# Performance work log

Measured on AMD Instinct MI355X. Metric: run time of the kernel, lower is better.

## Reference

```python
import jax, jax.numpy as jnp
import numpy as np
from jax import lax

B, T, D, E, N, P, S, NCLS, NBLK = 64, 16384, 128, 256, 8, 16, 1024, 18, 3
EPS = 1e-5


def setup_inputs() -> dict:
    key = jax.random.key(0)
    ks = jax.random.split(key, 20)
    inp = {
        'inputs': jax.random.normal(ks[0], (B, T, 6), jnp.float32),
        'acc_w': jax.random.normal(ks[1], (D // 2, 3, P), jnp.float32) * 0.1,
        'acc_b': jnp.zeros((D // 2,), jnp.float32),
        'gyro_w': jax.random.normal(ks[2], (D // 2, 3, P), jnp.float32) * 0.1,
        'gyro_b': jnp.zeros((D // 2,), jnp.float32),
        'pos_emb': jax.random.normal(ks[3], (S, D), jnp.float32),
        'ln_g': jnp.ones((NBLK, D), jnp.float32),
        'ln_b': jnp.zeros((NBLK, D), jnp.float32),
        'pc1_w': jax.random.normal(ks[4], (NBLK, E, D), jnp.float32) * 0.05,
        'pc1_b': jnp.zeros((NBLK, E), jnp.float32),
        'dw_w': jax.random.normal(ks[5], (NBLK, E, 5), jnp.float32) * 0.1,
        'dw_b': jnp.zeros((NBLK, E), jnp.float32),
        'bn_g': jnp.ones((NBLK, E), jnp.float32),
        'bn_b': jnp.zeros((NBLK, E), jnp.float32),
        'bn_mean': jnp.zeros((NBLK, E), jnp.float32),
        'bn_var': jnp.ones((NBLK, E), jnp.float32),
        'Ap': -0.5 * jnp.ones((NBLK, E), jnp.float32),
        'Bp': jax.random.normal(ks[6], (NBLK, E, N), jnp.float32) * 0.1,
        'Cp': jax.random.normal(ks[7], (NBLK, E, N), jnp.float32) * 0.1,
        'Dp': jax.random.normal(ks[8], (NBLK, E), jnp.float32) * 0.1,
        'pc2_w': jax.random.normal(ks[9], (NBLK, D, E), jnp.float32) * 0.05,
        'pc2_b': jnp.zeros((NBLK, D), jnp.float32),
        'fln_g': jnp.ones((D,), jnp.float32),
        'fln_b': jnp.zeros((D,), jnp.float32),
        'hw1': jax.random.normal(ks[10], (D, 2 * D), jnp.float32) * 0.05,
        'hb1': jnp.zeros((2 * D,), jnp.float32),
        'hw2': jax.random.normal(ks[11], (2 * D, NCLS), jnp.float32) * 0.05,
        'hb2': jnp.zeros((NCLS,), jnp.float32),
    }
    return inp


def _layernorm(x, g, b):
    m = x.mean(-1, keepdims=True)
    v = ((x - m) ** 2).mean(-1, keepdims=True)
    return (x - m) * lax.rsqrt(v + EPS) * g + b


def _conv1d(x, w, b, stride):
    # x [B,C,L], w [O,I,K]
    y = lax.conv_general_dilated(x, w, (stride,), 'VALID',
                                 dimension_numbers=('NCH', 'OIH', 'NCH'))
    return y + b[None, :, None]


def _mamba(x, pc1_w, pc1_b, dw_w, dw_b, bn_g, bn_b, bn_mean, bn_var,
           Ap, Bp, Cp, Dp, pc2_w, pc2_b):
    # x: [B,S,D]
    xc = jax.nn.silu(jnp.einsum('bsd,ed->bse', x, pc1_w) + pc1_b)  # [B,S,E]
    xt = jnp.swapaxes(xc, 1, 2)  # [B,E,S]
    # depthwise conv k=5, pad=2, groups=E
    xl = lax.conv_general_dilated(xt, dw_w[:, None, :], (1,), [(2, 2)],
                                  feature_group_count=E,
                                  dimension_numbers=('NCH', 'OIH', 'NCH'))
    xl = xl + dw_b[None, :, None]
    # BatchNorm1d (eval mode, running stats)
    scale = bn_g * lax.rsqrt(bn_var + EPS)
    xl = (xl - bn_mean[None, :, None]) * scale[None, :, None] + bn_b[None, :, None]
    xl = jax.nn.silu(xl)
    x_local = jnp.swapaxes(xl, 1, 2)  # [B,S,E]
    # SSM scan: h = exp(A)*h + x_t * B ; y = sum(C*h) + D*x_t
    A_exp = jnp.exp(Ap)  # [E]

    def step(h, xt_):
        # h [B,E,N], xt_ [B,E]
        h = A_exp[None, :, None] * h + xt_[..., None] * Bp[None]
        y = jnp.einsum('ben,en->be', h, Cp) + Dp * xt_
        return h, y

    h0 = jnp.zeros((x_local.shape[0], E, N), x_local.dtype)
    _, ys = lax.scan(step, h0, jnp.swapaxes(x_local, 0, 1))  # ys [S,B,E]
    out = jnp.swapaxes(ys, 0, 1)  # [B,S,E]
    out = jnp.einsum('bse,de->bsd', out, pc2_w) + pc2_b
    return out


def reference(inputs, acc_w, acc_b, gyro_w, gyro_b, pos_emb,
              ln_g, ln_b, pc1_w, pc1_b, dw_w, dw_b, bn_g, bn_b, bn_mean, bn_var,
              Ap, Bp, Cp, Dp, pc2_w, pc2_b, fln_g, fln_b, hw1, hb1, hw2, hb2):
    acc = jnp.swapaxes(inputs[:, :, :3], 1, 2)   # [B,3,T]
    gyro = jnp.swapaxes(inputs[:, :, 3:], 1, 2)  # [B,3,T]
    acc_p = jnp.swapaxes(_conv1d(acc, acc_w, acc_b, 16), 1, 2)    # [B,S,D/2]
    gyro_p = jnp.swapaxes(_conv1d(gyro, gyro_w, gyro_b, 16), 1, 2)
    x = jnp.concatenate([acc_p, gyro_p], axis=2)  # [B,S,D]
    x = x + pos_emb[None]
    for i in range(NBLK):
        y = _layernorm(x, ln_g[i], ln_b[i])
        y = _mamba(y, pc1_w[i], pc1_b[i], dw_w[i], dw_b[i], bn_g[i], bn_b[i],
                   bn_mean[i], bn_var[i], Ap[i], Bp[i], Cp[i], Dp[i],
                   pc2_w[i], pc2_b[i])
        x = y + x
    x = _layernorm(x, fln_g, fln_b)
    x = x.mean(axis=1)  # [B,D]
    h = jax.nn.silu(x @ hw1 + hb1)
    logits = h @ hw2 + hb2
    return jax.nn.softmax(logits, axis=-1)
```

## Files before the change

kernel.cpp:

```cpp
#include <hip/hip_runtime.h>
#include <hip/hip_bf16.h>

#define BB 64
#define TT 16384
#define DD 128
#define EE 256
#define NN 8
#define SS 1024
#define NCLS 18
#define NBLK 3
#define EPSV 1e-5f

typedef __bf16 bf16x8 __attribute__((ext_vector_type(8)));
typedef __bf16 bf16x4 __attribute__((ext_vector_type(4)));
typedef float f32x4 __attribute__((ext_vector_type(4)));
typedef unsigned short ushort_t;

__device__ __forceinline__ float silu_f(float z) {
    return z * __builtin_amdgcn_rcpf(1.0f + __expf(-z));
}
__device__ __forceinline__ unsigned int bfbits(float v) {
    return (unsigned int)__builtin_bit_cast(unsigned short, (__bf16)v);
}
__device__ __forceinline__ float bflow(unsigned int u) {
    return (float)__builtin_bit_cast(__bf16, (unsigned short)(u & 0xffffu));
}
__device__ __forceinline__ float bfhigh(unsigned int u) {
    return (float)__builtin_bit_cast(__bf16, (unsigned short)(u >> 16));
}

__global__ __launch_bounds__(256) void k_pack(
    const float* __restrict__ w1, const float* __restrict__ w2,
    const float* __restrict__ dw_w, const float* __restrict__ dw_b,
    const float* __restrict__ bn_g, const float* __restrict__ bn_b,
    const float* __restrict__ bn_mean, const float* __restrict__ bn_var,
    const float* __restrict__ Ap, const float* __restrict__ Bp,
    const float* __restrict__ Cp, const float* __restrict__ Dp,
    ushort_t* __restrict__ wpk1, ushort_t* __restrict__ wpk2,
    float* __restrict__ sparm) {
    const int t0 = blockIdx.x * 256 + threadIdx.x;
    if (t0 >= 24576) {
        const int t = t0 - 24576;
        if (t >= 768) return;
        const int le = t;
        const float scale = bn_g[le] * rsqrtf(bn_var[le] + EPSV);
        float cb = 0.0f;
#pragma unroll
        for (int n = 0; n < 8; ++n) cb += Cp[le * 8 + n] * Bp[le * 8 + n];
        float* dst = sparm + (size_t)le * 12;
        dst[0] = dw_w[le * 5 + 0] * scale;
        dst[1] = dw_w[le * 5 + 1] * scale;
        dst[2] = dw_w[le * 5 + 2] * scale;
        dst[3] = dw_w[le * 5 + 3] * scale;
        dst[4] = dw_w[le * 5 + 4] * scale;
        dst[5] = (dw_b[le] - bn_mean[le]) * scale + bn_b[le];
        dst[6] = __expf(Ap[le]);
        dst[7] = cb;
        dst[8] = Dp[le];
        dst[9] = 0.0f; dst[10] = 0.0f; dst[11] = 0.0f;
        return;
    }
    const float* src;
    uint4* dst;
    if (t0 < 12288) {
        const int L = t0 >> 12;
        const int r = t0 & 4095;
        const int ks = r >> 10;
        const int r2 = r & 1023;
        const int nf = r2 >> 6;
        const int lane = r2 & 63;
        const int col = nf * 16 + (lane & 15);
        const int k0 = ks * 32 + (lane >> 4) * 8;
        src = w1 + ((size_t)L * EE + col) * DD + k0;
        dst = (uint4*)wpk1 + t0;
    } else {
        const int t = t0 - 12288;
        const int L = t >> 12;
        const int r = t & 4095;
        const int ks = r >> 9;
        const int r2 = r & 511;
        const int nf = r2 >> 6;
        const int lane = r2 & 63;
        const int col = nf * 16 + (lane & 15);
        const int k0 = ks * 32 + (lane >> 4) * 8;
        src = w2 + ((size_t)L * DD + col) * EE + k0;
        dst = (uint4*)wpk2 + t;
    }
    const float4 a = ((const float4*)src)[0];
    const float4 b = ((const float4*)src)[1];
    bf16x8 pk;
    pk[0] = (__bf16)a.x; pk[1] = (__bf16)a.y; pk[2] = (__bf16)a.z; pk[3] = (__bf16)a.w;
    pk[4] = (__bf16)b.x; pk[5] = (__bf16)b.y; pk[6] = (__bf16)b.z; pk[7] = (__bf16)b.w;
    *dst = __builtin_bit_cast(uint4, pk);
}

__device__ __forceinline__ void xt_store(ushort_t* xt16, int row, int col,
                                         ushort_t val) {
    xt16[row * 128 + (((col >> 3) ^ (row & 7)) << 3) + (col & 7)] = val;
}

template <int MROWS, int NT>
__device__ __forceinline__ void ln_pc1_tail(
    char* smem, const int tid,
    const float* __restrict__ lng, const float* __restrict__ lnb,
    const ushort_t* __restrict__ wpk, const float* __restrict__ bias1,
    __bf16* __restrict__ xcT, const int bidx, const int sg0) {
    constexpr int TPR = NT / MROWS;
    constexpr int CPT = 16 / TPR;
    const uint4* xt = (const uint4*)smem;
    uint4* A2 = (uint4*)(smem + MROWS * 256);

    {
        const int row = tid / TPR;
        const int q = tid % TPR;
        float v[CPT * 8];
#pragma unroll
        for (int i = 0; i < CPT; ++i) {
            const uint4 tv4 = xt[row * 16 + ((q * CPT + i) ^ (row & 7))];
            const bf16x8 tv = __builtin_bit_cast(bf16x8, tv4);
#pragma unroll
            for (int e2 = 0; e2 < 8; ++e2) v[i * 8 + e2] = (float)tv[e2];
        }
        float s1 = 0.0f, s2 = 0.0f;
#pragma unroll
        for (int i = 0; i < CPT * 8; ++i) { s1 += v[i]; s2 += v[i] * v[i]; }
        s1 += __shfl_xor(s1, 1); s2 += __shfl_xor(s2, 1);
        s1 += __shfl_xor(s1, 2); s2 += __shfl_xor(s2, 2);
        const float mean = s1 * (1.0f / 128.0f);
        const float rstd = rsqrtf(s2 * (1.0f / 128.0f) - mean * mean + EPSV);
        const float4* gp4 = (const float4*)lng;
        const float4* bp4 = (const float4*)lnb;
#pragma unroll
        for (int c = 0; c < CPT; ++c) {
            const int ci = q * CPT + c;
            float4 g0 = gp4[ci * 2], g1 = gp4[ci * 2 + 1];
            float4 b0 = bp4[ci * 2], b1 = bp4[ci * 2 + 1];
            const float gg[8] = {g0.x, g0.y, g0.z, g0.w, g1.x, g1.y, g1.z, g1.w};
            const float bb2[8] = {b0.x, b0.y, b0.z, b0.w, b1.x, b1.y, b1.z, b1.w};
            bf16x8 pk;
#pragma unroll
            for (int e2 = 0; e2 < 8; ++e2)
                pk[e2] = (__bf16)((v[c * 8 + e2] - mean) * rstd * gg[e2] + bb2[e2]);
            A2[(row * 16 + ci) ^ (row & 7)] = __builtin_bit_cast(uint4, pk);
        }
    }
    __syncthreads();

    const int wv = tid >> 6;
    const int wr = wv >> 2;
    const int wc = wv & 3;
    const int lane = tid & 63;
    const int lrow = lane & 15;
    const int lk = lane >> 4;
    const uint4* wq = (const uint4*)wpk;

    f32x4 acc[4][4] = {};
    for (int ks = 0; ks < 4; ++ks) {
        bf16x8 av[4], bw[4];
#pragma unroll
        for (int m = 0; m < 4; ++m) {
            const int row = wr * 64 + m * 16 + lrow;
            const int idx = (row * 16 + ks * 4 + lk) ^ (row & 7);
            av[m] = __builtin_bit_cast(bf16x8, A2[idx]);
        }
#pragma unroll
        for (int n = 0; n < 4; ++n) {
            const int nf = wc * 4 + n;
            bw[n] = __builtin_bit_cast(bf16x8, wq[(ks * 16 + nf) * 64 + lane]);
        }
#pragma unroll
        for (int m = 0; m < 4; ++m)
#pragma unroll
            for (int n = 0; n < 4; ++n)
                acc[m][n] = __builtin_amdgcn_mfma_f32_16x16x32_bf16(av[m], bw[n], acc[m][n], 0, 0, 0);
    }

#pragma unroll
    for (int n = 0; n < 4; ++n) {
        const int col = wc * 64 + n * 16 + lrow;
        const float bv = bias1[col];
#pragma unroll
        for (int m = 0; m < 4; ++m) {
            bf16x4 pk;
#pragma unroll
            for (int r = 0; r < 4; ++r)
                pk[r] = (__bf16)silu_f(acc[m][n][r] + bv);
            const int sg = sg0 + wr * 8 + m * 2 + (lk >> 1);
            __bf16* dst = xcT + ((((size_t)bidx * 128 + sg) * EE + col) << 3) +
                          (lk & 1) * 4;
            *(bf16x4*)dst = pk;
        }
    }
}

__global__ __launch_bounds__(256) void k_stem_mfma(
    const float* __restrict__ in, const float* __restrict__ acc_w,
    const float* __restrict__ acc_b, const float* __restrict__ gyro_w,
    const float* __restrict__ gyro_b, const float* __restrict__ pos_emb,
    __bf16* __restrict__ x,
    const float* __restrict__ lng, const float* __restrict__ lnb,
    const ushort_t* __restrict__ wpk1, const float* __restrict__ pc1b,
    __bf16* __restrict__ xcT) {
    __shared__ __align__(16) char smem[49152];
    uint4* Wl = (uint4*)smem;
    uint4* Al = (uint4*)(smem + 32768);

    const int tid = threadIdx.x;
    const int rbase = blockIdx.x * 64;
    const int b = rbase >> 10;
    const int sbase = rbase & 1023;

    if (tid < 128) {
        const int d = tid;
        const float* wsrc = (d < 64) ? (acc_w + d * 48) : (gyro_w + (d - 64) * 48);
        float aw[48];
        const float4* wq4 = (const float4*)wsrc;
#pragma unroll
        for (int q = 0; q < 12; ++q) {
            float4 t = wq4[q];
            aw[q * 4 + 0] = t.x; aw[q * 4 + 1] = t.y;
            aw[q * 4 + 2] = t.z; aw[q * 4 + 3] = t.w;
        }
        const bool isacc = (d < 64);
#pragma unroll
        for (int cc = 0; cc < 12; ++cc) {
            unsigned int wb[8];
#pragma unroll
            for (int e = 0; e < 8; ++e) {
                const int j = cc * 8 + e;
                const int p = j / 6, rem = j % 6;
                float val;
                if (rem < 3) val = isacc ? aw[rem * 16 + p] : 0.0f;
                else         val = isacc ? 0.0f : aw[(rem - 3) * 16 + p];
                wb[e] = bfbits(val);
            }
            uint4 pk;
            pk.x = wb[0] | (wb[1] << 16);
            pk.y = wb[2] | (wb[3] << 16);
            pk.z = wb[4] | (wb[5] << 16);
            pk.w = wb[6] | (wb[7] << 16);
            Wl[d * 16 + (cc ^ (d & 7))] = pk;
        }
    }

    {
        const float* abase = in + (size_t)b * (TT * 6) + (size_t)sbase * 96;
#pragma unroll
        for (int it = 0; it < 3; ++it) {
            const int idx = it * 256 + tid;
            const int row = idx / 12;
            const int ch = idx % 12;
            const float* src = abase + row * 96 + ch * 8;
            const float4 t0 = *(const float4*)src;
            const float4 t1 = *(const float4*)(src + 4);
            uint4 pk;
            pk.x = bfbits(t0.x) | (bfbits(t0.y) << 16);
            pk.y = bfbits(t0.z) | (bfbits(t0.w) << 16);
            pk.z = bfbits(t1.x) | (bfbits(t1.y) << 16);
            pk.w = bfbits(t1.z) | (bfbits(t1.w) << 16);
            Al[row * 16 + (ch ^ (row & 7))] = pk;
        }
    }
    __syncthreads();

    const int wv = tid >> 6;
    const int lane = tid & 63;
    const int lrow = lane & 15;
    const int lk = lane >> 4;

    f32x4 acc[4][2] = {};
#pragma unroll
    for (int ks = 0; ks < 3; ++ks) {
        bf16x8 a[4], bf[2];
#pragma unroll
        for (int m = 0; m < 4; ++m) {
            const int row = m * 16 + lrow;
            a[m] = __builtin_bit_cast(bf16x8, Al[row * 16 + ((ks * 4 + lk) ^ (row & 7))]);
        }
#pragma unroll
        for (int n = 0; n < 2; ++n) {
            const int col = (wv * 2 + n) * 16 + lrow;
            bf[n] = __builtin_bit_cast(bf16x8, Wl[col * 16 + ((ks * 4 + lk) ^ (col & 7))]);
        }
#pragma unroll
        for (int m = 0; m < 4; ++m)
#pragma unroll
            for (int n = 0; n < 2; ++n)
                acc[m][n] = __builtin_amdgcn_mfma_f32_16x16x32_bf16(a[m], bf[n], acc[m][n], 0, 0, 0);
    }
    __syncthreads();

    ushort_t* xt16 = (ushort_t*)smem;
#pragma unroll
    for (int n = 0; n < 2; ++n) {
        const int col = (wv * 2 + n) * 16 + lrow;
        const float bv = (col < 64) ? acc_b[col] : gyro_b[col - 64];
#pragma unroll
        for (int m = 0; m < 4; ++m)
#pragma unroll
            for (int r = 0; r < 4; ++r) {
                const int row = m * 16 + lk * 4 + r;
                const float pe = pos_emb[(size_t)(sbase + row) * DD + col];
                const float xv = acc[m][n][r] + bv + pe;
                const __bf16 xb = (__bf16)xv;
                x[(size_t)(rbase + row) * DD + col] = xb;
                xt_store(xt16, row, col, __builtin_bit_cast(ushort_t, xb));
            }
    }
    __syncthreads();
    ln_pc1_tail<64, 256>(smem, tid, lng, lnb, wpk1, pc1b, xcT, b, sbase >> 3);
}

template <int TAIL>
__global__ __launch_bounds__(512, 4) void k_scan_pc2(
    const __bf16* __restrict__ xcIn,
    const ushort_t* __restrict__ wpk2_,
    const float* __restrict__ sparm,
    const float* __restrict__ bias, __bf16* __restrict__ x,
    const float* __restrict__ lng, const float* __restrict__ lnb,
    const ushort_t* __restrict__ wpk1, const float* __restrict__ pc1b,
    __bf16* __restrict__ xcOut) {
    __shared__ __align__(16) char smem[65536];

    const int tid = threadIdx.x;
    const int sc = blockIdx.x;
    const int b = blockIdx.y;

    {
        const int e = tid & 255;
        const int sub = tid >> 8;
        const int sce = sc * 2 + sub;
        const float4 p0 = *(const float4*)(sparm + (size_t)e * 12);
        const float4 p1 = *(const float4*)(sparm + (size_t)e * 12 + 4);
        const float Dv = sparm[(size_t)e * 12 + 8];
        const float d0 = p0.x, d1 = p0.y, d2 = p0.z, d3 = p0.w;
        const float d4 = p1.x, cbias = p1.y, Aexp = p1.z, cb = p1.w;

        const int sgbase = sce * 8 - 4;
        const uint4* xq = (const uint4*)xcIn + ((size_t)b * 128 + sgbase) * EE + e;
        uint4 G[13];
#pragma unroll
        for (int j = 0; j < 13; ++j) {
            const int sg = sgbase + j;
            G[j] = (sg >= 0 && sg < 128) ? xq[j * EE] : make_uint4(0, 0, 0, 0);
        }

        __bf16* lbase = (__bf16*)smem;
        const int ehash = e >> 3;
        const int elow = e & 7;
        const int rowoff = sub * 64;

        float g = 0.0f, pw6, pw7;
        if (sce != 0) {
            pw6 = bflow(G[0].w); pw7 = bfhigh(G[0].w);
#pragma unroll
            for (int j = 1; j <= 3; ++j) {
                float cw[8];
                cw[0] = bflow(G[j].x); cw[1] = bfhigh(G[j].x);
                cw[2] = bflow(G[j].y); cw[3] = bfhigh(G[j].y);
                cw[4] = bflow(G[j].z); cw[5] = bfhigh(G[j].z);
                cw[6] = bflow(G[j].w); cw[7] = bfhigh(G[j].w);
                const float nh0 = bflow(G[j + 1].x);
                const float nh1 = bfhigh(G[j + 1].x);
#pragma unroll
                for (int u = 0; u < 8; ++u) {
                    const float xm2 = (u >= 2) ? cw[u - 2] : (u == 0 ? pw6 : pw7);
                    const float xm1 = (u >= 1) ? cw[u - 1] : pw7;
                    const float x0 = cw[u];
                    const float xp1 = (u < 7) ? cw[u + 1] : nh0;
                    const float xp2 = (u < 6) ? cw[u + 2] : (u == 6 ? nh0 : nh1);
                    const float z = xm2 * d0 + xm1 * d1 + x0 * d2 + xp1 * d3 +
                                    xp2 * d4 + cbias;
                    g = fmaf(Aexp, g, silu_f(z));
                }
                pw6 = cw[6]; pw7 = cw[7];
            }
        } else {
            pw6 = 0.0f; pw7 = 0.0f;
        }

#pragma unroll
        for (int j = 4; j <= 11; ++j) {
            float cw[8];
            cw[0] = bflow(G[j].x); cw[1] = bfhigh(G[j].x);
            cw[2] = bflow(G[j].y); cw[3] = bfhigh(G[j].y);
            cw[4] = bflow(G[j].z); cw[5] = bfhigh(G[j].z);
            cw[6] = bflow(G[j].w); cw[7] = bfhigh(G[j].w);
            const float nh0 = bflow(G[j + 1].x);
            const float nh1 = bfhigh(G[j + 1].x);

            float aa[8];
#pragma unroll
            for (int u = 0; u < 8; ++u) {
                const float xm2 = (u >= 2) ? cw[u - 2] : (u == 0 ? pw6 : pw7);
                const float xm1 = (u >= 1) ? cw[u - 1] : pw7;
                const float x0 = cw[u];
                const float xp1 = (u < 7) ? cw[u + 1] : nh0;
                const float xp2 = (u < 6) ? cw[u + 2] : (u == 6 ? nh0 : nh1);
                const float z = xm2 * d0 + xm1 * d1 + x0 * d2 + xp1 * d3 +
                                xp2 * d4 + cbias;
                aa[u] = silu_f(z);
            }
#pragma unroll
            for (int u = 0; u < 8; ++u) {
                g = fmaf(Aexp, g, aa[u]);
                const int r = rowoff + (j - 4) * 8 + u;
                lbase[r * 256 + ((ehash ^ (r & 7)) << 3) + elow] =
                    (__bf16)(cb * g + Dv * aa[u]);
            }
            pw6 = cw[6]; pw7 = cw[7];
        }
    }
    __syncthreads();

    const size_t rbase = ((size_t)b << 10) + ((size_t)sc << 7);
    const int wv = tid >> 6;
    const int wr = wv >> 2;
    const int wc = wv & 3;
    const int lane = tid & 63;
    const int lrow = lane & 15;
    const int lk = lane >> 4;
    const uint4* wq = (const uint4*)wpk2_;
    const uint4* Albd = (const uint4*)smem;

    f32x4 acc[4][2] = {};
    for (int ks = 0; ks < 8; ++ks) {
        bf16x8 a[4], bfr[2];
#pragma unroll
        for (int m = 0; m < 4; ++m) {
            const int row = wr * 64 + m * 16 + lrow;
            const int idx = (row * 32 + ks * 4 + lk) ^ (row & 7);
            a[m] = __builtin_bit_cast(bf16x8, Albd[idx]);
        }
#pragma unroll
        for (int n = 0; n < 2; ++n) {
            const int nf = wc * 2 + n;
            bfr[n] = __builtin_bit_cast(bf16x8, wq[(ks * 8 + nf) * 64 + lane]);
        }
#pragma unroll
        for (int m = 0; m < 4; ++m)
#pragma unroll
            for (int n = 0; n < 2; ++n)
                acc[m][n] = __builtin_amdgcn_mfma_f32_16x16x32_bf16(a[m], bfr[n], acc[m][n], 0, 0, 0);
    }
    if constexpr (TAIL) __syncthreads();

    ushort_t* xt16 = (ushort_t*)smem;
#pragma unroll
    for (int n = 0; n < 2; ++n) {
        const int col = wc * 32 + n * 16 + lrow;
        const float bv = bias[col];
#pragma unroll
        for (int m = 0; m < 4; ++m)
#pragma unroll
            for (int r = 0; r < 4; ++r) {
                const int row = wr * 64 + m * 16 + lk * 4 + r;
                __bf16* xp = x + (rbase + row) * DD + col;
                const float xn = (float)*xp + acc[m][n][r] + bv;
                const __bf16 xb = (__bf16)xn;
                *xp = xb;
                if constexpr (TAIL)
                    xt_store(xt16, row, col, __builtin_bit_cast(ushort_t, xb));
            }
    }
    if constexpr (TAIL) {
        __syncthreads();
        ln_pc1_tail<128, 512>(smem, tid, lng, lnb, wpk1, pc1b, xcOut, b, sc * 16);
    }
}

__global__ __launch_bounds__(256) void k_finln_s1(
    const __bf16* __restrict__ x, float* __restrict__ partial) {
    const int chunk = blockIdx.x;
    const int b = blockIdx.y;
    const int tid = threadIdx.x;
    const int wv = tid >> 6;
    const int lane = tid & 63;
    const __bf16* xb = x + ((size_t)b * SS + chunk * 128) * DD;

    float a0 = 0.0f, a1 = 0.0f;
    for (int s = wv; s < 128; s += 4) {
        const unsigned int vv = *(const unsigned int*)(xb + (size_t)s * DD + lane * 2);
        const float vx = bflow(vv);
        const float vy = bfhigh(vv);
        float s1 = vx + vy;
        float s2 = vx * vx + vy * vy;
#pragma unroll
        for (int m = 1; m <= 32; m <<= 1) {
            s1 += __shfl_xor(s1, m);
            s2 += __shfl_xor(s2, m);
        }
        const float mean = s1 * (1.0f / 128.0f);
        const float rstd = rsqrtf(s2 * (1.0f / 128.0f) - mean * mean + EPSV);
        a0 += (vx - mean) * rstd;
        a1 += (vy - mean) * rstd;
    }
    __shared__ float red[4][128];
    red[wv][lane * 2] = a0;
    red[wv][lane * 2 + 1] = a1;
    __syncthreads();
    if (tid < 128) {
        partial[((size_t)b * 8 + chunk) * 128 + tid] =
            red[0][tid] + red[1][tid] + red[2][tid] + red[3][tid];
    }
}

__global__ __launch_bounds__(256) void k_head(
    const float* __restrict__ partial, const float* __restrict__ fg,
    const float* __restrict__ fb, const float* __restrict__ hw1,
    const float* __restrict__ hb1, const float* __restrict__ hw2,
    const float* __restrict__ hb2, float* __restrict__ out) {
    const int b = blockIdx.x;
    const int tid = threadIdx.x;
    __shared__ float xmb[128];
    __shared__ float hh[256];
    __shared__ float lg[18];
    __shared__ float eg[18];

    if (tid < 128) {
        float s = 0.0f;
#pragma unroll
        for (int c = 0; c < 8; ++c)
            s += partial[((size_t)b * 8 + c) * 128 + tid];
        xmb[tid] = fg[tid] * (s * (1.0f / (float)SS)) + fb[tid];
    }
    __syncthreads();

    float z = hb1[tid];
    for (int k = 0; k < 128; ++k) z += xmb[k] * hw1[k * 256 + tid];
    hh[tid] = z / (1.0f + expf(-z));
    __syncthreads();

    if (tid < NCLS) {
        float a = hb2[tid];
        for (int k = 0; k < 256; ++k) a += hh[k] * hw2[k * NCLS + tid];
        lg[tid] = a;
    }
    __syncthreads();
    if (tid < NCLS) {
        float m = lg[0];
        for (int j = 1; j < NCLS; ++j) m = fmaxf(m, lg[j]);
        eg[tid] = expf(lg[tid] - m);
    }
    __syncthreads();
    if (tid < NCLS) {
        float ssum = 0.0f;
        for (int j = 0; j < NCLS; ++j) ssum += eg[j];
        out[b * NCLS + tid] = eg[tid] / ssum;
    }
}

extern "C" void kernel_launch(void* const* d_in, const int* in_sizes, int n_in,
                              void* d_out, int out_size, void* d_ws, size_t ws_size,
                              hipStream_t stream) {
    const float* inputs  = (const float*)d_in[0];
    const float* acc_w   = (const float*)d_in[1];
    const float* acc_b   = (const float*)d_in[2];
    const float* gyro_w  = (const float*)d_in[3];
    const float* gyro_b  = (const float*)d_in[4];
    const float* pos_emb = (const float*)d_in[5];
    const float* ln_g    = (const float*)d_in[6];
    const float* ln_b    = (const float*)d_in[7];
    const float* pc1_w   = (const float*)d_in[8];
    const float* pc1_b   = (const float*)d_in[9];
    const float* dw_w    = (const float*)d_in[10];
    const float* dw_b    = (const float*)d_in[11];
    const float* bn_g    = (const float*)d_in[12];
    const float* bn_b    = (const float*)d_in[13];
    const float* bn_mean = (const float*)d_in[14];
    const float* bn_var  = (const float*)d_in[15];
    const float* Ap      = (const float*)d_in[16];
    const float* Bp      = (const float*)d_in[17];
    const float* Cp      = (const float*)d_in[18];
    const float* Dp      = (const float*)d_in[19];
    const float* pc2_w   = (const float*)d_in[20];
    const float* pc2_b   = (const float*)d_in[21];
    const float* fln_g   = (const float*)d_in[22];
    const float* fln_b   = (const float*)d_in[23];
    const float* hw1     = (const float*)d_in[24];
    const float* hb1     = (const float*)d_in[25];
    const float* hw2     = (const float*)d_in[26];
    const float* hb2     = (const float*)d_in[27];

    const size_t nx  = (size_t)BB * SS * DD;
    const size_t nxc = (size_t)BB * SS * EE;

    ushort_t* wsu = (ushort_t*)d_ws;
    ushort_t* xb   = wsu;
    ushort_t* xc0  = xb + nx;
    ushort_t* xc1  = xc0 + nxc;
    ushort_t* wpk1 = xc1 + nxc;
    ushort_t* wpk2 = wpk1 + 3 * 32768;
    float* sparm   = (float*)(wpk2 + 3 * 32768);
    float* partial = sparm + 3 * 256 * 12;

    __bf16* x    = (__bf16*)xb;
    __bf16* xcT0 = (__bf16*)xc0;
    __bf16* xcT1 = (__bf16*)xc1;

    k_pack<<<99, 256, 0, stream>>>(pc1_w, pc2_w, dw_w, dw_b, bn_g, bn_b,
                                   bn_mean, bn_var, Ap, Bp, Cp, Dp,
                                   wpk1, wpk2, sparm);

    k_stem_mfma<<<1024, 256, 0, stream>>>(inputs, acc_w, acc_b, gyro_w, gyro_b,
                                          pos_emb, x,
                                          ln_g, ln_b, wpk1, pc1_b, xcT0);

    k_scan_pc2<1><<<dim3(8, BB), 512, 0, stream>>>(
        xcT0, wpk2, sparm,
        pc2_b, x,
        ln_g + DD, ln_b + DD, wpk1 + 32768, pc1_b + EE, xcT1);

    k_scan_pc2<1><<<dim3(8, BB), 512, 0, stream>>>(
        xcT1, wpk2 + 32768, sparm + 256 * 12,
        pc2_b + DD, x,
        ln_g + 2 * DD, ln_b + 2 * DD, wpk1 + 2 * 32768, pc1_b + 2 * EE, xcT0);

    k_scan_pc2<0><<<dim3(8, BB), 512, 0, stream>>>(
        xcT0, wpk2 + 2 * 32768, sparm + 2 * 256 * 12,
        pc2_b + 2 * DD, x,
        nullptr, nullptr, nullptr, nullptr, nullptr);

    k_finln_s1<<<dim3(8, BB), 256, 0, stream>>>(x, partial);
    k_head<<<BB, 256, 0, stream>>>(partial, fln_g, fln_b, hw1, hb1, hw2, hb2,
                                   (float*)d_out);
}
```

Measured before the change: 153.8 us.

## Fuse per-layer LN, pc1, scan and pc2 into one kernel with recomputed halo

Each block now loads its 128-row chunk of x plus a 32-row halo, and computes layernorm and the pc1 GEMM itself. It then runs the depthwise conv and scan on pc1 output kept in shared memory, and applies pc2 with the residual, writing to a ping-pong x buffer. This removes the global xcT intermediate (B*S*E bf16 written and read per layer) and drops the LN/pc1 tail from the stem and previous layer. In exchange the halo rows are recomputed for pc1 and the scan warmup. Shared memory grows to about 124KB per block, which lowers occupancy, and the scan runs in serialized 32-row steps separated by barriers.

Result: slower. 257.6 us (+67.4%).

```diff
diff --git a/kernel.cpp b/kernel.cpp
--- a/kernel.cpp
+++ b/kernel.cpp
@@ -94,113 +94,11 @@
     *dst = __builtin_bit_cast(uint4, pk);
 }
 
-__device__ __forceinline__ void xt_store(ushort_t* xt16, int row, int col,
-                                         ushort_t val) {
-    xt16[row * 128 + (((col >> 3) ^ (row & 7)) << 3) + (col & 7)] = val;
-}
-
-template <int MROWS, int NT>
-__device__ __forceinline__ void ln_pc1_tail(
-    char* smem, const int tid,
-    const float* __restrict__ lng, const float* __restrict__ lnb,
-    const ushort_t* __restrict__ wpk, const float* __restrict__ bias1,
-    __bf16* __restrict__ xcT, const int bidx, const int sg0) {
-    constexpr int TPR = NT / MROWS;
-    constexpr int CPT = 16 / TPR;
-    const uint4* xt = (const uint4*)smem;
-    uint4* A2 = (uint4*)(smem + MROWS * 256);
-
-    {
-        const int row = tid / TPR;
-        const int q = tid % TPR;
-        float v[CPT * 8];
-#pragma unroll
-        for (int i = 0; i < CPT; ++i) {
-            const uint4 tv4 = xt[row * 16 + ((q * CPT + i) ^ (row & 7))];
-            const bf16x8 tv = __builtin_bit_cast(bf16x8, tv4);
-#pragma unroll
-            for (int e2 = 0; e2 < 8; ++e2) v[i * 8 + e2] = (float)tv[e2];
-        }
-        float s1 = 0.0f, s2 = 0.0f;
-#pragma unroll
-        for (int i = 0; i < CPT * 8; ++i) { s1 += v[i]; s2 += v[i] * v[i]; }
-        s1 += __shfl_xor(s1, 1); s2 += __shfl_xor(s2, 1);
-        s1 += __shfl_xor(s1, 2); s2 += __shfl_xor(s2, 2);
-        const float mean = s1 * (1.0f / 128.0f);
-        const float rstd = rsqrtf(s2 * (1.0f / 128.0f) - mean * mean + EPSV);
-        const float4* gp4 = (const float4*)lng;
-        const float4* bp4 = (const float4*)lnb;
-#pragma unroll
-        for (int c = 0; c < CPT; ++c) {
-            const int ci = q * CPT + c;
-            float4 g0 = gp4[ci * 2], g1 = gp4[ci * 2 + 1];
-            float4 b0 = bp4[ci * 2], b1 = bp4[ci * 2 + 1];
-            const float gg[8] = {g0.x, g0.y, g0.z, g0.w, g1.x, g1.y, g1.z, g1.w};
-            const float bb2[8] = {b0.x, b0.y, b0.z, b0.w, b1.x, b1.y, b1.z, b1.w};
-            bf16x8 pk;
-#pragma unroll
-            for (int e2 = 0; e2 < 8; ++e2)
-                pk[e2] = (__bf16)((v[c * 8 + e2] - mean) * rstd * gg[e2] + bb2[e2]);
-            A2[(row * 16 + ci) ^ (row & 7)] = __builtin_bit_cast(uint4, pk);
-        }
-    }
-    __syncthreads();
-
-    const int wv = tid >> 6;
-    const int wr = wv >> 2;
-    const int wc = wv & 3;
-    const int lane = tid & 63;
-    const int lrow = lane & 15;
-    const int lk = lane >> 4;
-    const uint4* wq = (const uint4*)wpk;
-
-    f32x4 acc[4][4] = {};
-    for (int ks = 0; ks < 4; ++ks) {
-        bf16x8 av[4], bw[4];
-#pragma unroll
-        for (int m = 0; m < 4; ++m) {
-            const int row = wr * 64 + m * 16 + lrow;
-            const int idx = (row * 16 + ks * 4 + lk) ^ (row & 7);
-            av[m] = __builtin_bit_cast(bf16x8, A2[idx]);
-        }
-#pragma unroll
-        for (int n = 0; n < 4; ++n) {
-            const int nf = wc * 4 + n;
-            bw[n] = __builtin_bit_cast(bf16x8, wq[(ks * 16 + nf) * 64 + lane]);
-        }
-#pragma unroll
-        for (int m = 0; m < 4; ++m)
-#pragma unroll
-            for (int n = 0; n < 4; ++n)
-                acc[m][n] = __builtin_amdgcn_mfma_f32_16x16x32_bf16(av[m], bw[n], acc[m][n], 0, 0, 0);
-    }
-
-#pragma unroll
-    for (int n = 0; n < 4; ++n) {
-        const int col = wc * 64 + n * 16 + lrow;
-        const float bv = bias1[col];
-#pragma unroll
-        for (int m = 0; m < 4; ++m) {
-            bf16x4 pk;
-#pragma unroll
-            for (int r = 0; r < 4; ++r)
-                pk[r] = (__bf16)silu_f(acc[m][n][r] + bv);
-            const int sg = sg0 + wr * 8 + m * 2 + (lk >> 1);
-            __bf16* dst = xcT + ((((size_t)bidx * 128 + sg) * EE + col) << 3) +
-                          (lk & 1) * 4;
-            *(bf16x4*)dst = pk;
-        }
-    }
-}
-
 __global__ __launch_bounds__(256) void k_stem_mfma(
     const float* __restrict__ in, const float* __restrict__ acc_w,
     const float* __restrict__ acc_b, const float* __restrict__ gyro_w,
     const float* __restrict__ gyro_b, const float* __restrict__ pos_emb,
-    __bf16* __restrict__ x,
-    const float* __restrict__ lng, const float* __restrict__ lnb,
-    const ushort_t* __restrict__ wpk1, const float* __restrict__ pc1b,
-    __bf16* __restrict__ xcT) {
+    __bf16* __restrict__ x) {
     __shared__ __align__(16) char smem[49152];
     uint4* Wl = (uint4*)smem;
     uint4* Al = (uint4*)(smem + 32768);
@@ -288,9 +186,7 @@
             for (int n = 0; n < 2; ++n)
                 acc[m][n] = __builtin_amdgcn_mfma_f32_16x16x32_bf16(a[m], bf[n], acc[m][n], 0, 0, 0);
     }
-    __syncthreads();
-
-    ushort_t* xt16 = (ushort_t*)smem;
+
 #pragma unroll
     for (int n = 0; n < 2; ++n) {
         const int col = (wv * 2 + n) * 16 + lrow;
@@ -301,171 +197,216 @@
             for (int r = 0; r < 4; ++r) {
                 const int row = m * 16 + lk * 4 + r;
                 const float pe = pos_emb[(size_t)(sbase + row) * DD + col];
-                const float xv = acc[m][n][r] + bv + pe;
-                const __bf16 xb = (__bf16)xv;
-                x[(size_t)(rbase + row) * DD + col] = xb;
-                xt_store(xt16, row, col, __builtin_bit_cast(ushort_t, xb));
-            }
-    }
-    __syncthreads();
-    ln_pc1_tail<64, 256>(smem, tid, lng, lnb, wpk1, pc1b, xcT, b, sbase >> 3);
-}
-
-template <int TAIL>
-__global__ __launch_bounds__(512, 4) void k_scan_pc2(
-    const __bf16* __restrict__ xcIn,
-    const ushort_t* __restrict__ wpk2_,
-    const float* __restrict__ sparm,
-    const float* __restrict__ bias, __bf16* __restrict__ x,
+                x[(size_t)(rbase + row) * DD + col] = (__bf16)(acc[m][n][r] + bv + pe);
+            }
+    }
+}
+
+__device__ __forceinline__ void pc2_quarter(
+    char* smem, const int q, const uint4* __restrict__ wq2,
+    const float* bv2, const __bf16* __restrict__ xOld,
+    __bf16* __restrict__ xNew, const int b, const int base,
+    const int wr, const int wc, const int lrow, const int lk, const int lane) {
+    const uint4* y4 = (const uint4*)(smem + 61440 + (q << 15));
+    f32x4 acc[2][2] = {};
+    for (int ks = 0; ks < 8; ++ks) {
+        bf16x8 a[2], bb[2];
+#pragma unroll
+        for (int m = 0; m < 2; ++m) {
+            const int row = wr * 32 + m * 16 + lrow;
+            a[m] = __builtin_bit_cast(bf16x8, y4[(row * 32 + ks * 4 + lk) ^ (row & 7)]);
+        }
+#pragma unroll
+        for (int n = 0; n < 2; ++n)
+            bb[n] = __builtin_bit_cast(bf16x8, wq2[(ks * 8 + wc * 2 + n) * 64 + lane]);
+#pragma unroll
+        for (int m = 0; m < 2; ++m)
+#pragma unroll
+            for (int n = 0; n < 2; ++n)
+                acc[m][n] = __builtin_amdgcn_mfma_f32_16x16x32_bf16(a[m], bb[n], acc[m][n], 0, 0, 0);
+    }
+#pragma unroll
+    for (int n = 0; n < 2; ++n) {
+        const int col = wc * 32 + n * 16 + lrow;
+#pragma unroll
+        for (int m = 0; m < 2; ++m)
+#pragma unroll
+            for (int r = 0; r < 4; ++r) {
+                const int row = wr * 32 + m * 16 + lk * 4 + r;
+                const size_t gp = ((size_t)b << 10) + base + (q << 6) + row;
+                const float old = (float)xOld[gp * DD + col];
+                xNew[gp * DD + col] = (__bf16)(old + acc[m][n][r] + bv2[n]);
+            }
+    }
+}
+
+__global__ __launch_bounds__(512, 2) void k_layer(
+    const __bf16* __restrict__ xOld, __bf16* __restrict__ xNew,
     const float* __restrict__ lng, const float* __restrict__ lnb,
     const ushort_t* __restrict__ wpk1, const float* __restrict__ pc1b,
-    __bf16* __restrict__ xcOut) {
-    __shared__ __align__(16) char smem[65536];
+    const float* __restrict__ sparm,
+    const ushort_t* __restrict__ wpk2, const float* __restrict__ pc2b) {
+    __shared__ __align__(16) char smem[126976];
+    uint4* xA4 = (uint4*)smem;
+    ushort_t* xcu = (ushort_t*)(smem + 45056);
 
     const int tid = threadIdx.x;
     const int sc = blockIdx.x;
     const int b = blockIdx.y;
+    const int base = sc << 7;
 
     {
-        const int e = tid & 255;
-        const int sub = tid >> 8;
-        const int sce = sc * 2 + sub;
-        const float4 p0 = *(const float4*)(sparm + (size_t)e * 12);
-        const float4 p1 = *(const float4*)(sparm + (size_t)e * 12 + 4);
-        const float Dv = sparm[(size_t)e * 12 + 8];
-        const float d0 = p0.x, d1 = p0.y, d2 = p0.z, d3 = p0.w;
-        const float d4 = p1.x, cbias = p1.y, Aexp = p1.z, cb = p1.w;
-
-        const int sgbase = sce * 8 - 4;
-        const uint4* xq = (const uint4*)xcIn + ((size_t)b * 128 + sgbase) * EE + e;
-        uint4 G[13];
-#pragma unroll
-        for (int j = 0; j < 13; ++j) {
-            const int sg = sgbase + j;
-            G[j] = (sg >= 0 && sg < 128) ? xq[j * EE] : make_uint4(0, 0, 0, 0);
-        }
-
-        __bf16* lbase = (__bf16*)smem;
-        const int ehash = e >> 3;
-        const int elow = e & 7;
-        const int rowoff = sub * 64;
-
-        float g = 0.0f, pw6, pw7;
-        if (sce != 0) {
-            pw6 = bflow(G[0].w); pw7 = bfhigh(G[0].w);
-#pragma unroll
-            for (int j = 1; j <= 3; ++j) {
-                float cw[8];
-                cw[0] = bflow(G[j].x); cw[1] = bfhigh(G[j].x);
-                cw[2] = bflow(G[j].y); cw[3] = bfhigh(G[j].y);
-                cw[4] = bflow(G[j].z); cw[5] = bfhigh(G[j].z);
-                cw[6] = bflow(G[j].w); cw[7] = bfhigh(G[j].w);
-                const float nh0 = bflow(G[j + 1].x);
-                const float nh1 = bfhigh(G[j + 1].x);
-#pragma unroll
-                for (int u = 0; u < 8; ++u) {
-                    const float xm2 = (u >= 2) ? cw[u - 2] : (u == 0 ? pw6 : pw7);
-                    const float xm1 = (u >= 1) ? cw[u - 1] : pw7;
-                    const float x0 = cw[u];
-                    const float xp1 = (u < 7) ? cw[u + 1] : nh0;
-                    const float xp2 = (u < 6) ? cw[u + 2] : (u == 6 ? nh0 : nh1);
-                    const float z = xm2 * d0 + xm1 * d1 + x0 * d2 + xp1 * d3 +
-                                    xp2 * d4 + cbias;
-                    g = fmaf(Aexp, g, silu_f(z));
+        const uint4* xO4 = (const uint4*)xOld;
+#pragma unroll
+        for (int k = 0; k < 6; ++k) {
+            const int c = k * 512 + tid;
+            if (c < 2816) {
+                const int row = c >> 4;
+                const int ch = c & 15;
+                const int rloc = base - 32 + row;
+                uint4 v = make_uint4(0, 0, 0, 0);
+                if ((unsigned)rloc < 1024u)
+                    v = xO4[((size_t)b * 1024 + rloc) * 16 + ch];
+                xA4[row * 16 + (ch ^ (row & 7))] = v;
+            }
+        }
+    }
+    __syncthreads();
+
+    {
+        const float4* gp4 = (const float4*)lng;
+        const float4* bp4 = (const float4*)lnb;
+#pragma unroll
+        for (int pass = 0; pass < 2; ++pass) {
+            const bool act = (pass == 0) || (tid < 192);
+            if (act) {
+                const int row = pass * 128 + (tid >> 2);
+                const int q = tid & 3;
+                float v[32];
+#pragma unroll
+                for (int i = 0; i < 4; ++i) {
+                    const uint4 tv4 = xA4[row * 16 + ((q * 4 + i) ^ (row & 7))];
+                    const bf16x8 tv = __builtin_bit_cast(bf16x8, tv4);
+#pragma unroll
+                    for (int e2 = 0; e2 < 8; ++e2) v[i * 8 + e2] = (float)tv[e2];
                 }
-                pw6 = cw[6]; pw7 = cw[7];
-            }
-        } else {
-            pw6 = 0.0f; pw7 = 0.0f;
-        }
-
-#pragma unroll
-        for (int j = 4; j <= 11; ++j) {
-            float cw[8];
-            cw[0] = bflow(G[j].x); cw[1] = bfhigh(G[j].x);
-            cw[2] = bflow(G[j].y); cw[3] = bfhigh(G[j].y);
-            cw[4] = bflow(G[j].z); cw[5] = bfhigh(G[j].z);
-            cw[6] = bflow(G[j].w); cw[7] = bfhigh(G[j].w);
-            const float nh0 = bflow(G[j + 1].x);
-            const float nh1 = bfhigh(G[j + 1].x);
-
-            float aa[8];
-#pragma unroll
-            for (int u = 0; u < 8; ++u) {
-                const float xm2 = (u >= 2) ? cw[u - 2] : (u == 0 ? pw6 : pw7);
-                const float xm1 = (u >= 1) ? cw[u - 1] : pw7;
-                const float x0 = cw[u];
-                const float xp1 = (u < 7) ? cw[u + 1] : nh0;
-                const float xp2 = (u < 6) ? cw[u + 2] : (u == 6 ? nh0 : nh1);
-                const float z = xm2 * d0 + xm1 * d1 + x0 * d2 + xp1 * d3 +
-                                xp2 * d4 + cbias;
-                aa[u] = silu_f(z);
-            }
-#pragma unroll
-            for (int u = 0; u < 8; ++u) {
-                g = fmaf(Aexp, g, aa[u]);
-                const int r = rowoff + (j - 4) * 8 + u;
-                lbase[r * 256 + ((ehash ^ (r & 7)) << 3) + elow] =
-                    (__bf16)(cb * g + Dv * aa[u]);
-            }
-            pw6 = cw[6]; pw7 = cw[7];
-        }
-    }
-    __syncthreads();
-
-    const size_t rbase = ((size_t)b << 10) + ((size_t)sc << 7);
+                float s1 = 0.0f, s2 = 0.0f;
+#pragma unroll
+                for (int i = 0; i < 32; ++i) { s1 += v[i]; s2 += v[i] * v[i]; }
+                s1 += __shfl_xor(s1, 1); s2 += __shfl_xor(s2, 1);
+                s1 += __shfl_xor(s1, 2); s2 += __shfl_xor(s2, 2);
+                const float mean = s1 * (1.0f / 128.0f);
+                const float rstd = rsqrtf(s2 * (1.0f / 128.0f) - mean * mean + EPSV);
+#pragma unroll
+                for (int ci = 0; ci < 4; ++ci) {
+                    const int ch = q * 4 + ci;
+                    float4 g0 = gp4[ch * 2], g1 = gp4[ch * 2 + 1];
+                    float4 b0 = bp4[ch * 2], b1 = bp4[ch * 2 + 1];
+                    const float gg[8] = {g0.x, g0.y, g0.z, g0.w, g1.x, g1.y, g1.z, g1.w};
+                    const float bb2[8] = {b0.x, b0.y, b0.z, b0.w, b1.x, b1.y, b1.z, b1.w};
+                    bf16x8 pk;
+#pragma unroll
+                    for (int e2 = 0; e2 < 8; ++e2)
+                        pk[e2] = (__bf16)((v[ci * 8 + e2] - mean) * rstd * gg[e2] + bb2[e2]);
+                    xA4[row * 16 + (ch ^ (row & 7))] = __builtin_bit_cast(uint4, pk);
+                }
+            }
+        }
+    }
+    __syncthreads();
+
     const int wv = tid >> 6;
-    const int wr = wv >> 2;
-    const int wc = wv & 3;
     const int lane = tid & 63;
     const int lrow = lane & 15;
     const int lk = lane >> 4;
-    const uint4* wq = (const uint4*)wpk2_;
-    const uint4* Albd = (const uint4*)smem;
-
-    f32x4 acc[4][2] = {};
-    for (int ks = 0; ks < 8; ++ks) {
-        bf16x8 a[4], bfr[2];
-#pragma unroll
-        for (int m = 0; m < 4; ++m) {
-            const int row = wr * 64 + m * 16 + lrow;
-            const int idx = (row * 32 + ks * 4 + lk) ^ (row & 7);
-            a[m] = __builtin_bit_cast(bf16x8, Albd[idx]);
-        }
-#pragma unroll
-        for (int n = 0; n < 2; ++n) {
-            const int nf = wc * 2 + n;
-            bfr[n] = __builtin_bit_cast(bf16x8, wq[(ks * 8 + nf) * 64 + lane]);
-        }
-#pragma unroll
-        for (int m = 0; m < 4; ++m)
-#pragma unroll
-            for (int n = 0; n < 2; ++n)
-                acc[m][n] = __builtin_amdgcn_mfma_f32_16x16x32_bf16(a[m], bfr[n], acc[m][n], 0, 0, 0);
-    }
-    if constexpr (TAIL) __syncthreads();
-
-    ushort_t* xt16 = (ushort_t*)smem;
-#pragma unroll
-    for (int n = 0; n < 2; ++n) {
-        const int col = wc * 32 + n * 16 + lrow;
-        const float bv = bias[col];
-#pragma unroll
-        for (int m = 0; m < 4; ++m)
-#pragma unroll
-            for (int r = 0; r < 4; ++r) {
-                const int row = wr * 64 + m * 16 + lk * 4 + r;
-                __bf16* xp = x + (rbase + row) * DD + col;
-                const float xn = (float)*xp + acc[m][n][r] + bv;
-                const __bf16 xb = (__bf16)xn;
-                *xp = xb;
-                if constexpr (TAIL)
-                    xt_store(xt16, row, col, __builtin_bit_cast(ushort_t, xb));
-            }
-    }
-    if constexpr (TAIL) {
+    const int wr = wv >> 2;
+    const int wc = wv & 3;
+    const uint4* wq1 = (const uint4*)wpk1;
+    const uint4* wq2 = (const uint4*)wpk2;
+
+    float bv1[4], bv2[2];
+#pragma unroll
+    for (int n = 0; n < 4; ++n) bv1[n] = pc1b[wc * 64 + n * 16 + lrow];
+#pragma unroll
+    for (int n = 0; n < 2; ++n) bv2[n] = pc2b[wc * 32 + n * 16 + lrow];
+
+    const int e = tid & 255;
+    const int sub = tid >> 8;
+    const float4 p0 = *(const float4*)(sparm + (size_t)e * 12);
+    const float4 p1 = *(const float4*)(sparm + (size_t)e * 12 + 4);
+    const float Dv = sparm[(size_t)e * 12 + 8];
+    const float d0 = p0.x, d1 = p0.y, d2 = p0.z, d3 = p0.w;
+    const float d4 = p1.x, cbias = p1.y, Aexp = p1.z, cb = p1.w;
+    const int cstart = sub ? 72 : ((sc == 0) ? 32 : 8);
+    const int cstore = sub ? 96 : 32;
+    const int Rlo = cstart - 2;
+    const int Rhi = sub ? 162 : 98;
+    const int ehash = e >> 3;
+    const int elow = e & 7;
+    float w0 = 0.0f, w1 = 0.0f, w2 = 0.0f, w3 = 0.0f, g = 0.0f;
+
+#pragma unroll
+    for (int rt = 0; rt < 6; ++rt) {
+        if (rt < 5 || wr == 0) {
+            f32x4 acc1[4] = {};
+            for (int ks = 0; ks < 4; ++ks) {
+                const int row = rt * 32 + wr * 16 + lrow;
+                const bf16x8 a = __builtin_bit_cast(
+                    bf16x8, xA4[row * 16 + ((ks * 4 + lk) ^ (row & 7))]);
+#pragma unroll
+                for (int n = 0; n < 4; ++n) {
+                    const bf16x8 bw = __builtin_bit_cast(
+                        bf16x8, wq1[(ks * 16 + wc * 4 + n) * 64 + lane]);
+                    acc1[n] = __builtin_amdgcn_mfma_f32_16x16x32_bf16(a, bw, acc1[n], 0, 0, 0);
+                }
+            }
+#pragma unroll
+            for (int n = 0; n < 4; ++n) {
+                const int col = wc * 64 + n * 16 + lrow;
+#pragma unroll
+                for (int r = 0; r < 4; ++r) {
+                    const int srow = wr * 16 + lk * 4 + r;
+                    const int rloc = base - 32 + rt * 32 + srow;
+                    float val = 0.0f;
+                    if ((unsigned)rloc < 1024u) val = silu_f(acc1[n][r] + bv1[n]);
+                    xcu[(srow * 512 + ((col << 1) ^ ((srow & 7) << 4))) >> 1] =
+                        __builtin_bit_cast(ushort_t, (__bf16)val);
+                }
+            }
+        }
         __syncthreads();
-        ln_pc1_tail<128, 512>(smem, tid, lng, lnb, wpk1, pc1b, xcOut, b, sc * 16);
+
+#pragma unroll
+        for (int i = 0; i < 32; ++i) {
+            const int R = rt * 32 + i;
+            if (R >= Rlo && R < Rhi) {
+                const ushort_t vu =
+                    xcu[(i * 512 + ((e << 1) ^ ((i & 7) << 4))) >> 1];
+                const float v = (float)__builtin_bit_cast(__bf16, vu);
+                const int c = R - 2;
+                if (c >= cstart) {
+                    const float z = w0 * d0 + w1 * d1 + w2 * d2 + w3 * d3 +
+                                    v * d4 + cbias;
+                    const float aa = silu_f(z);
+                    g = fmaf(Aexp, g, aa);
+                    if (c >= cstore) {
+                        const int p = c - 32;
+                        ushort_t* yb =
+                            (ushort_t*)(smem + 61440 + ((p >> 6) << 15));
+                        const int pl = p & 63;
+                        yb[pl * 256 + ((ehash ^ (pl & 7)) << 3) + elow] =
+                            __builtin_bit_cast(ushort_t, (__bf16)(cb * g + Dv * aa));
+                    }
+                }
+                w0 = w1; w1 = w2; w2 = w3; w3 = v;
+            }
+        }
+        __syncthreads();
+
+        if (rt == 3)
+            pc2_quarter(smem, 0, wq2, bv2, xOld, xNew, b, base, wr, wc, lrow, lk, lane);
+        if (rt == 5)
+            pc2_quarter(smem, 1, wq2, bv2, xOld, xNew, b, base, wr, wc, lrow, lk, lane);
     }
 }
 
@@ -582,46 +523,36 @@
     const float* hw2     = (const float*)d_in[26];
     const float* hb2     = (const float*)d_in[27];
 
-    const size_t nx  = (size_t)BB * SS * DD;
-    const size_t nxc = (size_t)BB * SS * EE;
+    const size_t nx = (size_t)BB * SS * DD;
 
     ushort_t* wsu = (ushort_t*)d_ws;
-    ushort_t* xb   = wsu;
-    ushort_t* xc0  = xb + nx;
-    ushort_t* xc1  = xc0 + nxc;
-    ushort_t* wpk1 = xc1 + nxc;
+    ushort_t* x1u  = wsu;
+    ushort_t* x2u  = x1u + nx;
+    ushort_t* wpk1 = x2u + nx;
     ushort_t* wpk2 = wpk1 + 3 * 32768;
     float* sparm   = (float*)(wpk2 + 3 * 32768);
     float* partial = sparm + 3 * 256 * 12;
 
-    __bf16* x    = (__bf16*)xb;
-    __bf16* xcT0 = (__bf16*)xc0;
-    __bf16* xcT1 = (__bf16*)xc1;
+    __bf16* x1 = (__bf16*)x1u;
+    __bf16* x2 = (__bf16*)x2u;
 
     k_pack<<<99, 256, 0, stream>>>(pc1_w, pc2_w, dw_w, dw_b, bn_g, bn_b,
                                    bn_mean, bn_var, Ap, Bp, Cp, Dp,
                                    wpk1, wpk2, sparm);
 
     k_stem_mfma<<<1024, 256, 0, stream>>>(inputs, acc_w, acc_b, gyro_w, gyro_b,
-                                          pos_emb, x,
-                                          ln_g, ln_b, wpk1, pc1_b, xcT0);
-
-    k_scan_pc2<1><<<dim3(8, BB), 512, 0, stream>>>(
-        xcT0, wpk2, sparm,
-        pc2_b, x,
-        ln_g + DD, ln_b + DD, wpk1 + 32768, pc1_b + EE, xcT1);
-
-    k_scan_pc2<1><<<dim3(8, BB), 512, 0, stream>>>(
-        xcT1, wpk2 + 32768, sparm + 256 * 12,
-        pc2_b + DD, x,
-        ln_g + 2 * DD, ln_b + 2 * DD, wpk1 + 2 * 32768, pc1_b + 2 * EE, xcT0);
-
-    k_scan_pc2<0><<<dim3(8, BB), 512, 0, stream>>>(
-        xcT0, wpk2 + 2 * 32768, sparm + 2 * 256 * 12,
-        pc2_b + 2 * DD, x,
-        nullptr, nullptr, nullptr, nullptr, nullptr);
-
-    k_finln_s1<<<dim3(8, BB), 256, 0, stream>>>(x, partial);
+                                          pos_emb, x1);
+
+    k_layer<<<dim3(8, BB), 512, 0, stream>>>(
+        x1, x2, ln_g, ln_b, wpk1, pc1_b, sparm, wpk2, pc2_b);
+    k_layer<<<dim3(8, BB), 512, 0, stream>>>(
+        x2, x1, ln_g + DD, ln_b + DD, wpk1 + 32768, pc1_b + EE,
+        sparm + 256 * 12, wpk2 + 32768, pc2_b + DD);
+    k_layer<<<dim3(8, BB), 512, 0, stream>>>(
+        x1, x2, ln_g + 2 * DD, ln_b + 2 * DD, wpk1 + 2 * 32768, pc1_b + 2 * EE,
+        sparm + 2 * 256 * 12, wpk2 + 2 * 32768, pc2_b + 2 * DD);
+
+    k_finln_s1<<<dim3(8, BB), 256, 0, stream>>>(x2, partial);
     k_head<<<BB, 256, 0, stream>>>(partial, fln_g, fln_b, hw1, hb1, hw2, hb2,
                                    (float*)d_out);
 }
```

## Split scan/pc2 blocks to 64-row chunks and vectorize stem x stores

Applied to the files above, without the earlier changes.

The scan+pc2 kernel now runs 256-thread blocks that each handle one 64-row chunk instead of two, doubling the grid to 16x64 blocks and halving shared memory per block. The intent is more resident blocks and better latency hiding, at the cost of more redundant halo loads per chunk. The stem kernel also stops writing x element-by-element from MFMA fragments. It instead writes x with coalesced 16-byte stores copied from the swizzled shared-memory tile.

New measurement: 154.4 us. Within noise of the previous version (+0.4%).

```diff
diff --git a/kernel.cpp b/kernel.cpp
--- a/kernel.cpp
+++ b/kernel.cpp
@@ -302,17 +302,27 @@
                 const int row = m * 16 + lk * 4 + r;
                 const float pe = pos_emb[(size_t)(sbase + row) * DD + col];
                 const float xv = acc[m][n][r] + bv + pe;
-                const __bf16 xb = (__bf16)xv;
-                x[(size_t)(rbase + row) * DD + col] = xb;
-                xt_store(xt16, row, col, __builtin_bit_cast(ushort_t, xb));
+                xt_store(xt16, row, col, __builtin_bit_cast(ushort_t, (__bf16)xv));
             }
     }
     __syncthreads();
+
+    {
+        uint4* xg = (uint4*)x;
+        const uint4* xt4 = (const uint4*)smem;
+#pragma unroll
+        for (int k = 0; k < 4; ++k) {
+            const int idx = k * 256 + tid;
+            const int row = idx >> 4;
+            const int ch = idx & 15;
+            xg[((size_t)(rbase + row) << 4) + ch] = xt4[row * 16 + (ch ^ (row & 7))];
+        }
+    }
     ln_pc1_tail<64, 256>(smem, tid, lng, lnb, wpk1, pc1b, xcT, b, sbase >> 3);
 }
 
 template <int TAIL>
-__global__ __launch_bounds__(512, 4) void k_scan_pc2(
+__global__ __launch_bounds__(256, 4) void k_scan_pc2(
     const __bf16* __restrict__ xcIn,
     const ushort_t* __restrict__ wpk2_,
     const float* __restrict__ sparm,
@@ -320,16 +330,14 @@
     const float* __restrict__ lng, const float* __restrict__ lnb,
     const ushort_t* __restrict__ wpk1, const float* __restrict__ pc1b,
     __bf16* __restrict__ xcOut) {
-    __shared__ __align__(16) char smem[65536];
+    __shared__ __align__(16) char smem[32768];
 
     const int tid = threadIdx.x;
-    const int sc = blockIdx.x;
+    const int sce = blockIdx.x;
     const int b = blockIdx.y;
 
     {
-        const int e = tid & 255;
-        const int sub = tid >> 8;
-        const int sce = sc * 2 + sub;
+        const int e = tid;
         const float4 p0 = *(const float4*)(sparm + (size_t)e * 12);
         const float4 p1 = *(const float4*)(sparm + (size_t)e * 12 + 4);
         const float Dv = sparm[(size_t)e * 12 + 8];
@@ -342,13 +350,13 @@
 #pragma unroll
         for (int j = 0; j < 13; ++j) {
             const int sg = sgbase + j;
-            G[j] = (sg >= 0 && sg < 128) ? xq[j * EE] : make_uint4(0, 0, 0, 0);
+            G[j] = (sg >= 0 && sg < 128) ? xq[(size_t)j * EE]
+                                         : make_uint4(0, 0, 0, 0);
         }
 
         __bf16* lbase = (__bf16*)smem;
         const int ehash = e >> 3;
         const int elow = e & 7;
-        const int rowoff = sub * 64;
 
         float g = 0.0f, pw6, pw7;
         if (sce != 0) {
@@ -404,7 +412,7 @@
 #pragma unroll
             for (int u = 0; u < 8; ++u) {
                 g = fmaf(Aexp, g, aa[u]);
-                const int r = rowoff + (j - 4) * 8 + u;
+                const int r = (j - 4) * 8 + u;
                 lbase[r * 256 + ((ehash ^ (r & 7)) << 3) + elow] =
                     (__bf16)(cb * g + Dv * aa[u]);
             }
@@ -413,10 +421,8 @@
     }
     __syncthreads();
 
-    const size_t rbase = ((size_t)b << 10) + ((size_t)sc << 7);
     const int wv = tid >> 6;
-    const int wr = wv >> 2;
-    const int wc = wv & 3;
+    const int wc = wv;
     const int lane = tid & 63;
     const int lrow = lane & 15;
     const int lk = lane >> 4;
@@ -428,7 +434,7 @@
         bf16x8 a[4], bfr[2];
 #pragma unroll
         for (int m = 0; m < 4; ++m) {
-            const int row = wr * 64 + m * 16 + lrow;
+            const int row = m * 16 + lrow;
             const int idx = (row * 32 + ks * 4 + lk) ^ (row & 7);
             a[m] = __builtin_bit_cast(bf16x8, Albd[idx]);
         }
@@ -445,6 +451,7 @@
     }
     if constexpr (TAIL) __syncthreads();
 
+    const size_t rbase = ((size_t)b << 10) + ((size_t)sce << 6);
     ushort_t* xt16 = (ushort_t*)smem;
 #pragma unroll
     for (int n = 0; n < 2; ++n) {
@@ -454,7 +461,7 @@
         for (int m = 0; m < 4; ++m)
 #pragma unroll
             for (int r = 0; r < 4; ++r) {
-                const int row = wr * 64 + m * 16 + lk * 4 + r;
+                const int row = m * 16 + lk * 4 + r;
                 __bf16* xp = x + (rbase + row) * DD + col;
                 const float xn = (float)*xp + acc[m][n][r] + bv;
                 const __bf16 xb = (__bf16)xn;
@@ -465,7 +472,7 @@
     }
     if constexpr (TAIL) {
         __syncthreads();
-        ln_pc1_tail<128, 512>(smem, tid, lng, lnb, wpk1, pc1b, xcOut, b, sc * 16);
+        ln_pc1_tail<64, 256>(smem, tid, lng, lnb, wpk1, pc1b, xcOut, b, sce * 8);
     }
 }
 
@@ -606,17 +613,17 @@
                                           pos_emb, x,
                                           ln_g, ln_b, wpk1, pc1_b, xcT0);
 
-    k_scan_pc2<1><<<dim3(8, BB), 512, 0, stream>>>(
+    k_scan_pc2<1><<<dim3(16, BB), 256, 0, stream>>>(
         xcT0, wpk2, sparm,
         pc2_b, x,
         ln_g + DD, ln_b + DD, wpk1 + 32768, pc1_b + EE, xcT1);
 
-    k_scan_pc2<1><<<dim3(8, BB), 512, 0, stream>>>(
+    k_scan_pc2<1><<<dim3(16, BB), 256, 0, stream>>>(
         xcT1, wpk2 + 32768, sparm + 256 * 12,
         pc2_b + DD, x,
         ln_g + 2 * DD, ln_b + 2 * DD, wpk1 + 2 * 32768, pc1_b + 2 * EE, xcT0);
 
-    k_scan_pc2<0><<<dim3(8, BB), 512, 0, stream>>>(
+    k_scan_pc2<0><<<dim3(16, BB), 256, 0, stream>>>(
         xcT0, wpk2 + 2 * 32768, sparm + 2 * 256 * 12,
         pc2_b + 2 * DD, x,
         nullptr, nullptr, nullptr, nullptr, nullptr);
```
